# Kernel tuning notes

Measured on AMD Instinct MI355X. Metric: run time of the kernel, lower is better.

Reference implementation:

```python
import jax, jax.numpy as jnp
import numpy as np

B, D, S = 16384, 1024, 1024

def _layernorm(x, g, b, eps=1e-5):
    mu = jnp.mean(x, axis=-1, keepdims=True)
    var = jnp.mean(jnp.square(x - mu), axis=-1, keepdims=True)
    return (x - mu) * jax.lax.rsqrt(var + eps) * g + b

def setup_inputs() -> dict:
    key = jax.random.key(0)
    ks = jax.random.split(key, 8)
    inv = lambda n: 1.0 / np.sqrt(n)
    return {
        "x": jax.random.normal(ks[0], (B, D), jnp.float32),
        "s_prev0": jax.random.normal(ks[1], (B, S), jnp.float32),
        "s_prev1": jax.random.normal(ks[2], (B, S), jnp.float32),
        "Wi": jax.random.uniform(ks[3], (4 * S, D), jnp.float32, -inv(D), inv(D)),
        "Ws": jax.random.uniform(ks[4], (4 * S, 2 * S), jnp.float32, -inv(2 * S), inv(2 * S)),
        "lni_g": jnp.ones((4 * S,), jnp.float32),
        "lni_b": jnp.zeros((4 * S,), jnp.float32),
        "lns_g": jnp.ones((4 * S,), jnp.float32),
        "lns_b": jnp.zeros((4 * S,), jnp.float32),
        "lnh_g": jnp.ones((S,), jnp.float32),
        "lnh_b": jnp.zeros((S,), jnp.float32),
    }

def reference(x, s_prev0, s_prev1, Wi, Ws, lni_g, lni_b, lns_g, lns_b, lnh_g, lnh_b):
    s = jnp.concatenate([s_prev0, s_prev1], axis=-1)  # [B, 2S]
    igates = _layernorm(x @ Wi.T, lni_g, lni_b)        # [B, 4S]
    sgates = _layernorm(s @ Ws.T, lns_g, lns_b)        # [B, 4S]
    gates = igates + sgates
    r_inv, i, n, l = jnp.split(gates, 4, axis=1)
    s_n = sgates[:, 2 * S:3 * S]
    l = jax.nn.sigmoid(l)
    r_inv = jax.nn.sigmoid(r_inv)
    i = jax.nn.sigmoid(i)
    n = jnp.tanh(n - r_inv * s_n)
    h = n + i * (l * s_prev0 + (1.0 - l) * s_prev1 - n)
    return _layernorm(h, lnh_g, lnh_b)
```

## Files before the change

### kernel.cpp

```cpp
#include <hip/hip_runtime.h>
#include <cstdint>


typedef unsigned short ushort_t;
typedef __attribute__((ext_vector_type(8))) __bf16 bf16x8;
typedef __attribute__((ext_vector_type(4))) float f32x4;

__device__ __forceinline__ ushort_t f2b(float f) {
    unsigned u = __float_as_uint(f);
    unsigned r = (u + 0x7fffu + ((u >> 16) & 1u)) >> 16;
    return (ushort_t)r;
}
__device__ __forceinline__ float b2f(ushort_t u) {
    return __uint_as_float(((unsigned)u) << 16);
}

__device__ __forceinline__ void gl_lds16(const void* g, void* l) {
    __builtin_amdgcn_global_load_lds(
        (const __attribute__((address_space(1))) unsigned int*)(uintptr_t)g,
        (__attribute__((address_space(3))) unsigned int*)(uintptr_t)l,
        16, 0, 0);
}

#define LOG2E 1.4426950408889634f
__device__ __forceinline__ float fexp2(float x) { return __builtin_amdgcn_exp2f(x); }
__device__ __forceinline__ float frcp(float x)  { return __builtin_amdgcn_rcpf(x); }
__device__ __forceinline__ float fsigmoid(float x) {
    return frcp(1.f + fexp2(-LOG2E * x));
}
__device__ __forceinline__ float ftanh(float y) {
    return 1.f - 2.f * frcp(1.f + fexp2((2.f * LOG2E) * y));
}

__global__ __launch_bounds__(256) void cast_bf16(const float* __restrict__ src,
                                                 ushort_t* __restrict__ dst, long n) {
    long i = ((long)blockIdx.x * 256 + threadIdx.x) * 4;
    if (i + 3 < n) {
        float4 v = *(const float4*)(src + i);
        ushort4 u;
        u.x = f2b(v.x); u.y = f2b(v.y); u.z = f2b(v.z); u.w = f2b(v.w);
        *(ushort4*)(dst + i) = u;
    }
}

__global__ __launch_bounds__(256) void cast_concat(const float* __restrict__ s0,
                                                   const float* __restrict__ s1,
                                                   ushort_t* __restrict__ dst) {
    long i = ((long)blockIdx.x * 256 + threadIdx.x) * 4;
    long row = i >> 11;
    int  col = (int)(i & 2047);
    const float* src = (col < 1024) ? (s0 + row * 1024 + col)
                                    : (s1 + row * 1024 + (col - 1024));
    float4 v = *(const float4*)src;
    ushort4 u;
    u.x = f2b(v.x); u.y = f2b(v.y); u.z = f2b(v.z); u.w = f2b(v.w);
    *(ushort4*)(dst + i) = u;
}

__global__ __launch_bounds__(256, 2) void gemm_bt(const ushort_t* __restrict__ A,
                                                  const ushort_t* __restrict__ W,
                                                  ushort_t* __restrict__ C,
                                                  int M, int N, int K) {
    __shared__ __align__(16) ushort_t As[2][128 * 32];
    __shared__ __align__(16) ushort_t Bs[2][128 * 32];

    const int t    = threadIdx.x;
    const int lane = t & 63;
    const int wave = t >> 6;
    const int wm   = (wave >> 1) * 64;
    const int wn   = (wave & 1) * 64;

    const int bm0 = blockIdx.y * 128;
    const int bn0 = blockIdx.x * 128;

    const int sr = t >> 2;
    const int sc = (t & 3) * 8;
    const ushort_t* Ag = A + (long)(bm0 + sr) * K + sc;
    const ushort_t* Wg = W + (long)(bn0 + sr) * K + sc;

    f32x4 acc[4][4];
#pragma unroll
    for (int i = 0; i < 4; i++)
#pragma unroll
        for (int j = 0; j < 4; j++) acc[i][j] = (f32x4){0.f, 0.f, 0.f, 0.f};

    const int mrow = lane & 15;
    const int kgrp = (lane >> 4) * 8;

    for (int k0 = 0; k0 < K; k0 += 64) {
#pragma unroll
        for (int h = 0; h < 2; h++) {
            int kh = k0 + h * 32;
            gl_lds16(Ag + kh,                As[h] + t * 8);
            gl_lds16(Ag + (long)64 * K + kh, As[h] + 2048 + t * 8);
            gl_lds16(Wg + kh,                Bs[h] + t * 8);
            gl_lds16(Wg + (long)64 * K + kh, Bs[h] + 2048 + t * 8);
        }
        __syncthreads();

#pragma unroll
        for (int h = 0; h < 2; h++) {
            bf16x8 af[4], bfr[4];
#pragma unroll
            for (int i = 0; i < 4; i++)
                af[i] = *(const bf16x8*)&As[h][(wm + i * 16 + mrow) * 32 + kgrp];
#pragma unroll
            for (int j = 0; j < 4; j++)
                bfr[j] = *(const bf16x8*)&Bs[h][(wn + j * 16 + mrow) * 32 + kgrp];
#pragma unroll
            for (int i = 0; i < 4; i++)
#pragma unroll
                for (int j = 0; j < 4; j++)
                    acc[i][j] = __builtin_amdgcn_mfma_f32_16x16x32_bf16(af[i], bfr[j], acc[i][j], 0, 0, 0);
        }
        __syncthreads();
    }

    const int quad = lane >> 4;
#pragma unroll
    for (int i = 0; i < 4; i++)
#pragma unroll
        for (int j = 0; j < 4; j++)
#pragma unroll
            for (int r = 0; r < 4; r++) {
                int cm = bm0 + wm + i * 16 + quad * 4 + r;
                int cn = bn0 + wn + j * 16 + (lane & 15);
                C[(long)cm * N + cn] = f2b(acc[i][j][r]);
            }
}

__global__ __launch_bounds__(256) void fuse_ln(const ushort_t* __restrict__ M1,
                                               const ushort_t* __restrict__ M2,
                                               const float* __restrict__ p0,
                                               const float* __restrict__ p1,
                                               const float* __restrict__ lni_g,
                                               const float* __restrict__ lni_b,
                                               const float* __restrict__ lns_g,
                                               const float* __restrict__ lns_b,
                                               const float* __restrict__ lnh_g,
                                               const float* __restrict__ lnh_b,
                                               float* __restrict__ out) {
    const int row = blockIdx.x;
    const int t   = threadIdx.x;
    const long base = (long)row * 4096;

    __shared__ float sred[16];
    __shared__ float stats[8];

    float v1[4][4], v2[4][4];
    float s1 = 0.f, q1 = 0.f, s2 = 0.f, q2 = 0.f;
#pragma unroll
    for (int q = 0; q < 4; q++) {
        ushort4 a = *(const ushort4*)(M1 + base + q * 1024 + t * 4);
        ushort4 b = *(const ushort4*)(M2 + base + q * 1024 + t * 4);
        const ushort_t* ap = (const ushort_t*)&a;
        const ushort_t* bp = (const ushort_t*)&b;
#pragma unroll
        for (int j = 0; j < 4; j++) {
            float f1 = b2f(ap[j]); v1[q][j] = f1; s1 += f1; q1 += f1 * f1;
            float f2 = b2f(bp[j]); v2[q][j] = f2; s2 += f2; q2 += f2 * f2;
        }
    }
    float r4[4] = {s1, q1, s2, q2};
#pragma unroll
    for (int off = 32; off > 0; off >>= 1) {
#pragma unroll
        for (int i = 0; i < 4; i++) r4[i] += __shfl_down(r4[i], off, 64);
    }
    if ((t & 63) == 0) {
        int w = t >> 6;
#pragma unroll
        for (int i = 0; i < 4; i++) sred[w * 4 + i] = r4[i];
    }
    __syncthreads();
    if (t == 0) {
        float S1 = 0, Q1 = 0, S2 = 0, Q2 = 0;
        for (int w = 0; w < 4; w++) {
            S1 += sred[w * 4]; Q1 += sred[w * 4 + 1];
            S2 += sred[w * 4 + 2]; Q2 += sred[w * 4 + 3];
        }
        float mu1 = S1 * (1.f / 4096.f), mu2 = S2 * (1.f / 4096.f);
        float var1 = Q1 * (1.f / 4096.f) - mu1 * mu1;
        float var2 = Q2 * (1.f / 4096.f) - mu2 * mu2;
        stats[0] = mu1; stats[1] = rsqrtf(var1 + 1e-5f);
        stats[2] = mu2; stats[3] = rsqrtf(var2 + 1e-5f);
    }
    __syncthreads();
    const float mu1 = stats[0], rs1 = stats[1], mu2 = stats[2], rs2 = stats[3];

    float4 Gi[4], Bi[4], Gs[4], Bs[4];
#pragma unroll
    for (int q = 0; q < 4; q++) {
        Gi[q] = *(const float4*)(lni_g + q * 1024 + t * 4);
        Bi[q] = *(const float4*)(lni_b + q * 1024 + t * 4);
        Gs[q] = *(const float4*)(lns_g + q * 1024 + t * 4);
        Bs[q] = *(const float4*)(lns_b + q * 1024 + t * 4);
    }
    float4 P0 = *(const float4*)(p0 + (long)row * 1024 + t * 4);
    float4 P1 = *(const float4*)(p1 + (long)row * 1024 + t * 4);

    float h[4];
    float sh = 0.f, qh = 0.f;
#pragma unroll
    for (int j = 0; j < 4; j++) {
        float gq[4], snv = 0.f;
#pragma unroll
        for (int q = 0; q < 4; q++) {
            float a = (v1[q][j] - mu1) * rs1 * ((const float*)&Gi[q])[j] + ((const float*)&Bi[q])[j];
            float b = (v2[q][j] - mu2) * rs2 * ((const float*)&Gs[q])[j] + ((const float*)&Bs[q])[j];
            if (q == 2) snv = b;
            gq[q] = a + b;
        }
        float rg = fsigmoid(gq[0]);
        float ig = fsigmoid(gq[1]);
        float lg = fsigmoid(gq[3]);
        float ng = ftanh(gq[2] - rg * snv);
        float pp0 = ((const float*)&P0)[j], pp1 = ((const float*)&P1)[j];
        float hv = ng + ig * (lg * pp0 + (1.f - lg) * pp1 - ng);
        h[j] = hv; sh += hv; qh += hv * hv;
    }
    float r2[2] = {sh, qh};
#pragma unroll
    for (int off = 32; off > 0; off >>= 1) {
#pragma unroll
        for (int i = 0; i < 2; i++) r2[i] += __shfl_down(r2[i], off, 64);
    }
    if ((t & 63) == 0) {
        int w = t >> 6;
        sred[w * 4] = r2[0]; sred[w * 4 + 1] = r2[1];
    }
    __syncthreads();
    if (t == 0) {
        float S = 0, Q = 0;
        for (int w = 0; w < 4; w++) { S += sred[w * 4]; Q += sred[w * 4 + 1]; }
        float mu = S * (1.f / 1024.f);
        float var = Q * (1.f / 1024.f) - mu * mu;
        stats[4] = mu; stats[5] = rsqrtf(var + 1e-5f);
    }
    __syncthreads();
    const float muh = stats[4], rsh = stats[5];

    float4 Gh = *(const float4*)(lnh_g + t * 4);
    float4 Bh = *(const float4*)(lnh_b + t * 4);
    float4 O;
#pragma unroll
    for (int j = 0; j < 4; j++)
        ((float*)&O)[j] = (h[j] - muh) * rsh * ((const float*)&Gh)[j] + ((const float*)&Bh)[j];
    *(float4*)(out + (long)row * 1024 + t * 4) = O;
}

extern "C" void kernel_launch(void* const* d_in, const int* in_sizes, int n_in,
                              void* d_out, int out_size, void* d_ws, size_t ws_size,
                              hipStream_t stream) {
    const float* x     = (const float*)d_in[0];
    const float* s0    = (const float*)d_in[1];
    const float* s1    = (const float*)d_in[2];
    const float* Wi    = (const float*)d_in[3];
    const float* Ws    = (const float*)d_in[4];
    const float* lni_g = (const float*)d_in[5];
    const float* lni_b = (const float*)d_in[6];
    const float* lns_g = (const float*)d_in[7];
    const float* lns_b = (const float*)d_in[8];
    const float* lnh_g = (const float*)d_in[9];
    const float* lnh_b = (const float*)d_in[10];
    float* out = (float*)d_out;

    char* wsb = (char*)d_ws;
    ushort_t* M1  = (ushort_t*)wsb;
    ushort_t* M2  = (ushort_t*)(wsb + (((size_t)128) << 20));
    ushort_t* Wsb = (ushort_t*)wsb;
    ushort_t* sb  = (ushort_t*)d_out;
    ushort_t* xb  = (ushort_t*)d_out;
    ushort_t* Wib = (ushort_t*)((char*)d_out + (((size_t)32) << 20));

    dim3 g(4096 / 128, 16384 / 128);

    cast_concat<<<32768, 256, 0, stream>>>(s0, s1, sb);
    cast_bf16<<<8192, 256, 0, stream>>>(Ws, Wsb, (long)4096 * 2048);
    gemm_bt<<<g, 256, 0, stream>>>(sb, Wsb, M2, 16384, 4096, 2048);
    cast_bf16<<<16384, 256, 0, stream>>>(x, xb, (long)16384 * 1024);
    cast_bf16<<<4096, 256, 0, stream>>>(Wi, Wib, (long)4096 * 1024);
    gemm_bt<<<g, 256, 0, stream>>>(xb, Wib, M1, 16384, 4096, 1024);
    fuse_ln<<<16384, 256, 0, stream>>>(M1, M2, s0, s1, lni_g, lni_b, lns_g,
                                       lns_b, lnh_g, lnh_b, out);
}
```

Measured before the change: 770.2 us.

## Rewrite bf16 GEMM with 256x256 tiles, swizzled LDS, and staged prefetch pipeline

Replaces the 128x128, 256-thread GEMM with a 256x256-tile, 512-thread kernel using 64-wide K steps, XOR-swizzled LDS layout, and a two-deep prefetch schedule that issues global-to-LDS loads in quarters interleaved with MFMA work. It also remaps workgroup IDs across XCD chiplets and uses setprio and fine-grained barriers with vmcnt waits. The intent is higher arithmetic intensity per tile, fewer LDS bank conflicts, and overlap of loads with matrix math. The costs are 128KB of LDS per block with launch_bounds(512,2), which may limit occupancy, and complex wait-count logic that is fragile.

New measurement: 889.9 us. +15.5%, slower.

```diff
diff --git a/kernel.cpp b/kernel.cpp
--- a/kernel.cpp
+++ b/kernel.cpp
@@ -57,76 +57,164 @@
     *(ushort4*)(dst + i) = u;
 }
 
-__global__ __launch_bounds__(256, 2) void gemm_bt(const ushort_t* __restrict__ A,
+
+__device__ __forceinline__ void stage2(const char* s0, const char* s1,
+                                       int d0, int d1, char* ldsbase,
+                                       int kt, int NT) {
+    if (kt < NT) {
+        long kb = (long)kt << 7;
+        char* lb = ldsbase + ((kt & 1) << 15);
+        gl_lds16(s0 + kb, lb + d0);
+        gl_lds16(s1 + kb, lb + d1);
+    }
+}
+
+__global__ __launch_bounds__(512, 2) void gemm_bt(const ushort_t* __restrict__ A,
                                                   const ushort_t* __restrict__ W,
                                                   ushort_t* __restrict__ C,
                                                   int M, int N, int K) {
-    __shared__ __align__(16) ushort_t As[2][128 * 32];
-    __shared__ __align__(16) ushort_t Bs[2][128 * 32];
-
+    (void)M;
+    __shared__ __align__(16) ushort_t As[2][256 * 64];
+    __shared__ __align__(16) ushort_t Bs[2][256 * 64];
+
+    const int NT   = K >> 6;
     const int t    = threadIdx.x;
     const int lane = t & 63;
-    const int wave = t >> 6;
-    const int wm   = (wave >> 1) * 64;
-    const int wn   = (wave & 1) * 64;
-
-    const int bm0 = blockIdx.y * 128;
-    const int bn0 = blockIdx.x * 128;
-
-    const int sr = t >> 2;
-    const int sc = (t & 3) * 8;
-    const ushort_t* Ag = A + (long)(bm0 + sr) * K + sc;
-    const ushort_t* Wg = W + (long)(bn0 + sr) * K + sc;
-
-    f32x4 acc[4][4];
-#pragma unroll
-    for (int i = 0; i < 4; i++)
-#pragma unroll
-        for (int j = 0; j < 4; j++) acc[i][j] = (f32x4){0.f, 0.f, 0.f, 0.f};
-
-    const int mrow = lane & 15;
-    const int kgrp = (lane >> 4) * 8;
-
-    for (int k0 = 0; k0 < K; k0 += 64) {
-#pragma unroll
-        for (int h = 0; h < 2; h++) {
-            int kh = k0 + h * 32;
-            gl_lds16(Ag + kh,                As[h] + t * 8);
-            gl_lds16(Ag + (long)64 * K + kh, As[h] + 2048 + t * 8);
-            gl_lds16(Wg + kh,                Bs[h] + t * 8);
-            gl_lds16(Wg + (long)64 * K + kh, Bs[h] + 2048 + t * 8);
+    const int w    = t >> 6;
+    const int gm   = w >> 2;
+    const int gn   = w & 3;
+    const int gb   = gn & 1;
+    const int wm   = gm << 7;
+    const int wn   = gn << 6;
+
+    const int nwg  = gridDim.x;
+    const int cpx  = nwg >> 3;
+    const int orig = blockIdx.x;
+    const int wgid = (orig & 7) * cpx + (orig >> 3);
+    const int NXB  = N >> 8;
+    const int bx   = wgid % NXB;
+    const int by   = wgid / NXB;
+    const int bm0  = by << 8;
+    const int bn0  = bx << 8;
+
+    const int u0r = t >> 3;
+    const int chb = (t & 7) << 4;
+    const int ur0 = u0r, ur1 = 64 + u0r;
+    const int cb0 = chb ^ (((ur0 >> 2) & 1) << 5);
+    const int cb1 = chb ^ (((ur1 >> 2) & 1) << 5);
+
+    #define AER(ur) ((ur) < 64 ? (ur) : (ur) + 128)
+    #define ALR(ur) ((ur) + 64)
+    #define BER(ur) (((((ur) >> 5) >> 1) << 7) + ((((ur) >> 5) & 1) * 96) + ((ur) & 31))
+    #define BLR(ur) ((ur) + 32 + (((ur) >> 6) << 6))
+
+    const char* sAe0 = (const char*)(A + (long)(bm0 + AER(ur0)) * K) + cb0;
+    const char* sAe1 = (const char*)(A + (long)(bm0 + AER(ur1)) * K) + cb1;
+    const char* sAl0 = (const char*)(A + (long)(bm0 + ALR(ur0)) * K) + cb0;
+    const char* sAl1 = (const char*)(A + (long)(bm0 + ALR(ur1)) * K) + cb1;
+    const char* sBe0 = (const char*)(W + (long)(bn0 + BER(ur0)) * K) + cb0;
+    const char* sBe1 = (const char*)(W + (long)(bn0 + BER(ur1)) * K) + cb1;
+    const char* sBl0 = (const char*)(W + (long)(bn0 + BLR(ur0)) * K) + cb0;
+    const char* sBl1 = (const char*)(W + (long)(bn0 + BLR(ur1)) * K) + cb1;
+
+    const int dAe0 = AER(ur0) * 128 + chb, dAe1 = AER(ur1) * 128 + chb;
+    const int dAl0 = ALR(ur0) * 128 + chb, dAl1 = ALR(ur1) * 128 + chb;
+    const int dBe0 = BER(ur0) * 128 + chb, dBe1 = BER(ur1) * 128 + chb;
+    const int dBl0 = BLR(ur0) * 128 + chb, dBl1 = BLR(ur1) * 128 + chb;
+
+    char* Abase = (char*)&As[0][0];
+    char* Bbase = (char*)&Bs[0][0];
+
+    const int ml   = lane & 15;
+    const int sb   = ((lane >> 2) & 1) << 5;
+    const int kc0  = ((lane >> 4) << 4) ^ sb;
+    const int kc1  = (64 + ((lane >> 4) << 4)) ^ sb;
+    const int arow = (wm + ml) << 7;
+    const int brow = (wn + ml) << 7;
+
+    f32x4 acc[4][4][2];
+#pragma unroll
+    for (int q = 0; q < 4; q++)
+#pragma unroll
+        for (int ii = 0; ii < 4; ii++)
+#pragma unroll
+            for (int jj = 0; jj < 2; jj++)
+                acc[q][ii][jj] = (f32x4){0.f, 0.f, 0.f, 0.f};
+
+    stage2(sBe0, sBe1, dBe0, dBe1, Bbase, 0, NT);
+    stage2(sAe0, sAe1, dAe0, dAe1, Abase, 0, NT);
+    stage2(sAl0, sAl1, dAl0, dAl1, Abase, 0, NT);
+    stage2(sBl0, sBl1, dBl0, dBl1, Bbase, 0, NT);
+    stage2(sBe0, sBe1, dBe0, dBe1, Bbase, 1, NT);
+    stage2(sAe0, sAe1, dAe0, dAe1, Abase, 1, NT);
+    asm volatile("s_waitcnt vmcnt(4)" ::: "memory");
+    __builtin_amdgcn_s_barrier();
+
+    for (int kt = 0; kt < NT; ++kt) {
+        const char* Ab = Abase + ((kt & 1) << 15);
+        const char* Bb = Bbase + ((kt & 1) << 15);
+#pragma unroll
+        for (int q = 0; q < 4; ++q) {
+            const int qm = (q & 1) ^ gm;
+            const int qn = (q >> 1) ^ gb;
+
+            bf16x8 af[4][2], bfr[2][2];
+#pragma unroll
+            for (int ii = 0; ii < 4; ii++) {
+                const int ro = arow + ((qm << 2) + ii) * 2048;
+                af[ii][0] = *(const bf16x8*)(Ab + ro + kc0);
+                af[ii][1] = *(const bf16x8*)(Ab + ro + kc1);
+            }
+#pragma unroll
+            for (int jj = 0; jj < 2; jj++) {
+                const int ro = brow + ((qn << 1) + jj) * 2048;
+                bfr[jj][0] = *(const bf16x8*)(Bb + ro + kc0);
+                bfr[jj][1] = *(const bf16x8*)(Bb + ro + kc1);
+            }
+
+            if (q == 0)      stage2(sAl0, sAl1, dAl0, dAl1, Abase, kt + 1, NT);
+            else if (q == 1) stage2(sBl0, sBl1, dBl0, dBl1, Bbase, kt + 1, NT);
+            else if (q == 2) stage2(sBe0, sBe1, dBe0, dBe1, Bbase, kt + 2, NT);
+            else             stage2(sAe0, sAe1, dAe0, dAe1, Abase, kt + 2, NT);
+
+            if (q == 3) {
+                if (kt < NT - 2) asm volatile("s_waitcnt vmcnt(4)" ::: "memory");
+                else             asm volatile("s_waitcnt vmcnt(0)" ::: "memory");
+            }
+            __builtin_amdgcn_s_barrier();
+            asm volatile("s_waitcnt lgkmcnt(0)" ::: "memory");
+            __builtin_amdgcn_sched_barrier(0);
+            __builtin_amdgcn_s_setprio(1);
+#pragma unroll
+            for (int kh = 0; kh < 2; kh++)
+#pragma unroll
+                for (int ii = 0; ii < 4; ii++)
+#pragma unroll
+                    for (int jj = 0; jj < 2; jj++)
+                        acc[q][ii][jj] = __builtin_amdgcn_mfma_f32_16x16x32_bf16(
+                            af[ii][kh], bfr[jj][kh], acc[q][ii][jj], 0, 0, 0);
+            __builtin_amdgcn_s_setprio(0);
+            __builtin_amdgcn_sched_barrier(0);
+            __builtin_amdgcn_s_barrier();
         }
-        __syncthreads();
-
-#pragma unroll
-        for (int h = 0; h < 2; h++) {
-            bf16x8 af[4], bfr[4];
-#pragma unroll
-            for (int i = 0; i < 4; i++)
-                af[i] = *(const bf16x8*)&As[h][(wm + i * 16 + mrow) * 32 + kgrp];
-#pragma unroll
-            for (int j = 0; j < 4; j++)
-                bfr[j] = *(const bf16x8*)&Bs[h][(wn + j * 16 + mrow) * 32 + kgrp];
-#pragma unroll
-            for (int i = 0; i < 4; i++)
-#pragma unroll
-                for (int j = 0; j < 4; j++)
-                    acc[i][j] = __builtin_amdgcn_mfma_f32_16x16x32_bf16(af[i], bfr[j], acc[i][j], 0, 0, 0);
-        }
-        __syncthreads();
-    }
-
-    const int quad = lane >> 4;
-#pragma unroll
-    for (int i = 0; i < 4; i++)
-#pragma unroll
-        for (int j = 0; j < 4; j++)
-#pragma unroll
-            for (int r = 0; r < 4; r++) {
-                int cm = bm0 + wm + i * 16 + quad * 4 + r;
-                int cn = bn0 + wn + j * 16 + (lane & 15);
-                C[(long)cm * N + cn] = f2b(acc[i][j][r]);
-            }
+    }
+
+    const int quad = (lane >> 4) << 2;
+#pragma unroll
+    for (int q = 0; q < 4; ++q) {
+        const int qm = (q & 1) ^ gm;
+        const int qn = (q >> 1) ^ gb;
+#pragma unroll
+        for (int ii = 0; ii < 4; ii++)
+#pragma unroll
+            for (int jj = 0; jj < 2; jj++)
+#pragma unroll
+                for (int r = 0; r < 4; r++) {
+                    const int cm = bm0 + wm + ((qm << 2) + ii) * 16 + quad + r;
+                    const int cn = bn0 + wn + ((qn << 1) + jj) * 16 + ml;
+                    C[(long)cm * N + cn] = f2b(acc[q][ii][jj][r]);
+                }
+    }
 }
 
 __global__ __launch_bounds__(256) void fuse_ln(const ushort_t* __restrict__ M1,
@@ -273,14 +361,14 @@
     ushort_t* xb  = (ushort_t*)d_out;
     ushort_t* Wib = (ushort_t*)((char*)d_out + (((size_t)32) << 20));
 
-    dim3 g(4096 / 128, 16384 / 128);
+    dim3 g(1024);
 
     cast_concat<<<32768, 256, 0, stream>>>(s0, s1, sb);
     cast_bf16<<<8192, 256, 0, stream>>>(Ws, Wsb, (long)4096 * 2048);
-    gemm_bt<<<g, 256, 0, stream>>>(sb, Wsb, M2, 16384, 4096, 2048);
+    gemm_bt<<<g, 512, 0, stream>>>(sb, Wsb, M2, 16384, 4096, 2048);
     cast_bf16<<<16384, 256, 0, stream>>>(x, xb, (long)16384 * 1024);
     cast_bf16<<<4096, 256, 0, stream>>>(Wi, Wib, (long)4096 * 1024);
-    gemm_bt<<<g, 256, 0, stream>>>(xb, Wib, M1, 16384, 4096, 1024);
+    gemm_bt<<<g, 512, 0, stream>>>(xb, Wib, M1, 16384, 4096, 1024);
     fuse_ln<<<16384, 256, 0, stream>>>(M1, M2, s0, s1, lni_g, lni_b, lns_g,
                                        lns_b, lnh_g, lnh_b, out);
 }
```
